# Performance work log

Hardware: AMD Instinct MI355X
Metric: run time of the kernel (lower is better)

## Reference

```python
import jax, jax.numpy as jnp
import numpy as np

B, S, D, H = 8, 1024, 1024, 16
DEPTH = D // H  # 64


def setup_inputs() -> dict:
    key = jax.random.key(0)
    ks = jax.random.split(key, 12)
    s = 1.0 / np.sqrt(D)
    return {
        "Q": jax.random.normal(ks[0], (B, S, D), jnp.float32),
        "K": jax.random.normal(ks[1], (B, S, D), jnp.float32),
        "V": jax.random.normal(ks[2], (B, S, D), jnp.float32),
        "mask": jnp.zeros((B, 1, 1, S), jnp.float32),
        "Wq": jax.random.normal(ks[3], (D, D), jnp.float32) * s,
        "bq": jnp.zeros((D,), jnp.float32),
        "Wk": jax.random.normal(ks[4], (D, D), jnp.float32) * s,
        "bk": jnp.zeros((D,), jnp.float32),
        "Wv": jax.random.normal(ks[5], (D, D), jnp.float32) * s,
        "bv": jnp.zeros((D,), jnp.float32),
        "Wo": jax.random.normal(ks[6], (D, D), jnp.float32) * s,
        "bo": jnp.zeros((D,), jnp.float32),
    }


def _split_heads(x):
    # [B,S,D] -> [B,H,S,depth]
    b, s, _ = x.shape
    return x.reshape(b, s, H, DEPTH).transpose(0, 2, 1, 3)


def reference(Q, K, V, mask, Wq, bq, Wk, bk, Wv, bv, Wo, bo):
    q = _split_heads(Q @ Wq + bq)  # [B,H,S,depth]
    k = _split_heads(K @ Wk + bk)
    v = _split_heads(V @ Wv + bv)
    scale = 1.0 / jnp.sqrt(jnp.asarray(DEPTH, q.dtype))
    scores = jnp.einsum('bhqd,bhkd->bhqk', q, k) * scale  # [B,H,Sq,Sk]
    scores = scores + mask * (-1e9)
    attn = jax.nn.softmax(scores, axis=-1)
    out = jnp.einsum('bhqk,bhkd->bhqd', attn, v)  # [B,H,S,depth]
    out = out.transpose(0, 2, 1, 3).reshape(Q.shape[0], Q.shape[1], D)
    out = out @ Wo + bo
    return out, attn
```

## Files before the change

kernel.cpp:

```cpp
#include <hip/hip_runtime.h>

#define Bb 8
#define Ss 1024
#define Dd 1024
#define Hh 16
#define BSD (Bb*Ss*Dd)
#define DDn (Dd*Dd)

typedef __bf16 bf16x8 __attribute__((ext_vector_type(8)));
typedef float  f32x4  __attribute__((ext_vector_type(4)));

__device__ __forceinline__ unsigned short f2bf(float f){
  unsigned u = __float_as_uint(f);
  u = (u + 0x7fffu + ((u >> 16) & 1u)) >> 16;
  return (unsigned short)u;
}
__device__ __forceinline__ float fexp2(float x){ return __builtin_exp2f(x); }

__device__ __forceinline__ void gload16(const ushort* g, ushort* l){
  __builtin_amdgcn_global_load_lds(
      (const __attribute__((address_space(1))) void*)g,
      (__attribute__((address_space(3))) void*)l, 16, 0, 0);
}

__global__ __launch_bounds__(256) void cvt_bf16(const float4* __restrict__ in,
                                                ushort4* __restrict__ out, int n4){
  int i = blockIdx.x*256 + threadIdx.x;
  if (i >= n4) return;
  float4 v = in[i];
  ushort4 o; o.x = f2bf(v.x); o.y = f2bf(v.y); o.z = f2bf(v.z); o.w = f2bf(v.w);
  out[i] = o;
}

__global__ __launch_bounds__(256) void transpose_w(const float* __restrict__ W,
                                                   ushort* __restrict__ WT){
  __shared__ float tl[32][33];
  int tx = threadIdx.x, ty = threadIdx.y;
  int bx = blockIdx.x*32, by = blockIdx.y*32;
  #pragma unroll
  for (int i=0;i<32;i+=8) tl[ty+i][tx] = W[(by+ty+i)*Dd + bx+tx];
  __syncthreads();
  #pragma unroll
  for (int i=0;i<32;i+=8) WT[(bx+ty+i)*Dd + by+tx] = f2bf(tl[tx][ty+i]);
}

__global__ __launch_bounds__(512) void transpose_v(const ushort* __restrict__ vh,
                                                   ushort* __restrict__ vt){
  __shared__ ushort tl[64][65];
  int tx = threadIdx.x, ty = threadIdx.y;
  long base = (long)blockIdx.y * 65536;
  int s0 = blockIdx.x*64;
  #pragma unroll
  for (int i=0;i<64;i+=8) tl[ty+i][tx] = vh[base + (long)(s0+ty+i)*64 + tx];
  __syncthreads();
  #pragma unroll
  for (int i=0;i<64;i+=8) vt[base + (long)(ty+i)*1024 + s0 + tx] = tl[tx][ty+i];
}

enum { M_PROJ=0, M_FINAL=3 };

template<int MODE>
__global__ __launch_bounds__(256) void gemm128(
    const ushort* __restrict__ A, const ushort* __restrict__ B,
    float* __restrict__ outf, ushort* __restrict__ outh,
    const float* __restrict__ aux)
{
  __shared__ __align__(16) ushort As[128*32];
  __shared__ __align__(16) ushort Bs[128*32];
  const int t = threadIdx.x, lane = t & 63, wave = t >> 6;
  const int m0 = blockIdx.x*128, n0 = blockIdx.y*128;
  const int wm = (wave>>1)*64, wn = (wave&1)*64;
  const int q = lane>>4, l16 = lane&15;
  const int row0 = t>>2, cc = (t&3)*8;

  ushort* lA0 = As + wave*512;
  ushort* lA1 = As + 2048 + wave*512;
  ushort* lB0 = Bs + wave*512;
  ushort* lB1 = Bs + 2048 + wave*512;
  const ushort* gA0 = A + (long)(m0+row0)*Dd + cc;
  const ushort* gA1 = A + (long)(m0+row0+64)*Dd + cc;
  const ushort* gB0 = B + (long)(n0+row0)*Dd + cc;
  const ushort* gB1 = B + (long)(n0+row0+64)*Dd + cc;

  f32x4 acc[4][4] = {};

  for (int k0=0; k0<Dd; k0+=32){
    __syncthreads();
    gload16(gA0+k0, lA0);
    gload16(gA1+k0, lA1);
    gload16(gB0+k0, lB0);
    gload16(gB1+k0, lB1);
    __syncthreads();
    bf16x8 af[4], bfr[4];
    #pragma unroll
    for (int i=0;i<4;i++){
      af[i]  = *(const bf16x8*)(As + (wm+i*16+l16)*32 + q*8);
      bfr[i] = *(const bf16x8*)(Bs + (wn+i*16+l16)*32 + q*8);
    }
    #pragma unroll
    for (int mi=0;mi<4;mi++)
    #pragma unroll
    for (int nj=0;nj<4;nj++)
      acc[mi][nj] = __builtin_amdgcn_mfma_f32_16x16x32_bf16(af[mi],bfr[nj],acc[mi][nj],0,0,0);
  }

  #pragma unroll
  for (int mi=0;mi<4;mi++)
  #pragma unroll
  for (int nj=0;nj<4;nj++)
  #pragma unroll
  for (int r=0;r<4;r++){
    float v = acc[mi][nj][r];
    const int row = m0 + wm + mi*16 + q*4 + r;
    const int col = n0 + wn + nj*16 + l16;
    v += aux[col];
    if (MODE == M_PROJ){
      const int b = row>>10, s = row&1023, h = col>>6, d = col&63;
      outh[((long)((b*Hh + h)*Ss + s)<<6) + d] = f2bf(v);
    } else {
      outf[(long)row*Dd + col] = v;
    }
  }
}

__global__ __launch_bounds__(256) void attn_fused(
    const ushort* __restrict__ qh,
    const ushort* __restrict__ kh,
    const ushort* __restrict__ vt,
    const float*  __restrict__ mask,
    float* __restrict__ attn_f,
    ushort* __restrict__ concat)
{
  __shared__ __align__(16) ushort qs[64][72];
  __shared__ __align__(16) ushort ks[64][72];
  __shared__ __align__(16) ushort vs[64][72];
  __shared__ __align__(16) ushort ps[64][72];
  __shared__ float msk[64];
  __shared__ float red_m[2][64];
  __shared__ float red_l[2][64];

  const int z = blockIdx.z;
  const int b = z >> 4, h = z & 15;
  const int t = threadIdx.x;
  const int lane = t & 63, wave = t >> 6;
  const int wm = (wave >> 1) * 32;
  const int wc = wave & 1;
  const int wn = wc * 32;
  const int q = lane >> 4, l16 = lane & 15;
  const int srow = t >> 2, sc = (t & 3) * 8;

  const ushort* qz = qh + ((long)z << 16);
  const ushort* kz = kh + ((long)z << 16);
  const ushort* vz = vt + ((long)z << 16);
  const int q0 = blockIdx.x * 64;
  const float LOG2E = 1.44269504f;
  const float SC2   = 0.125f * LOG2E;
  const float MSC2  = -1e9f * LOG2E;

  {
    const ushort* src = qz + (long)(q0 + srow) * 64 + sc;
    *(uint4*)(&qs[srow][sc])      = *(const uint4*)(src);
    *(uint4*)(&qs[srow][sc + 32]) = *(const uint4*)(src + 32);
  }

  float m2[2], lsum[2];
  m2[0] = m2[1] = -1e30f; lsum[0] = lsum[1] = 0.f;

  uint4 kv0, kv1; float mv;
  {
    const ushort* ksrc = kz + (long)srow * 64 + sc;
    kv0 = *(const uint4*)(ksrc); kv1 = *(const uint4*)(ksrc + 32);
    mv = (t < 64) ? mask[(b<<10) + t] * MSC2 : 0.f;
  }
  for (int s = 0; s < 16; ++s){
    __syncthreads();
    *(uint4*)(&ks[srow][sc])      = kv0;
    *(uint4*)(&ks[srow][sc + 32]) = kv1;
    if (t < 64) msk[t] = mv;
    __syncthreads();
    if (s < 15){
      const ushort* ksrc = kz + (long)((s+1)*64 + srow) * 64 + sc;
      kv0 = *(const uint4*)(ksrc); kv1 = *(const uint4*)(ksrc + 32);
      if (t < 64) mv = mask[(b<<10) + (s+1)*64 + t] * MSC2;
    }

    f32x4 accs[2][2] = {};
    #pragma unroll
    for (int kk=0; kk<2; ++kk){
      bf16x8 a0 = *(const bf16x8*)(&ks[wm      + l16][kk*32 + q*8]);
      bf16x8 a1 = *(const bf16x8*)(&ks[wm + 16 + l16][kk*32 + q*8]);
      bf16x8 b0 = *(const bf16x8*)(&qs[wn      + l16][kk*32 + q*8]);
      bf16x8 b1 = *(const bf16x8*)(&qs[wn + 16 + l16][kk*32 + q*8]);
      accs[0][0] = __builtin_amdgcn_mfma_f32_16x16x32_bf16(a0,b0,accs[0][0],0,0,0);
      accs[0][1] = __builtin_amdgcn_mfma_f32_16x16x32_bf16(a0,b1,accs[0][1],0,0,0);
      accs[1][0] = __builtin_amdgcn_mfma_f32_16x16x32_bf16(a1,b0,accs[1][0],0,0,0);
      accs[1][1] = __builtin_amdgcn_mfma_f32_16x16x32_bf16(a1,b1,accs[1][1],0,0,0);
    }
    #pragma unroll
    for (int tj=0; tj<2; ++tj){
      float sv[8];
      #pragma unroll
      for (int ti=0; ti<2; ++ti)
      #pragma unroll
      for (int r=0; r<4; ++r){
        const int key = wm + ti*16 + q*4 + r;
        sv[ti*4+r] = accs[ti][tj][r]*SC2 + msk[key];
      }
      float mx01 = fmaxf(sv[0],sv[1]), mx23 = fmaxf(sv[2],sv[3]);
      float mx45 = fmaxf(sv[4],sv[5]), mx67 = fmaxf(sv[6],sv[7]);
      float mx = fmaxf(fmaxf(fmaxf(mx01,mx23), fmaxf(mx45,mx67)), m2[tj]);
      float e0 = fexp2(sv[0]-mx), e1 = fexp2(sv[1]-mx);
      float e2 = fexp2(sv[2]-mx), e3 = fexp2(sv[3]-mx);
      float e4 = fexp2(sv[4]-mx), e5 = fexp2(sv[5]-mx);
      float e6 = fexp2(sv[6]-mx), e7 = fexp2(sv[7]-mx);
      float add = ((e0+e1)+(e2+e3)) + ((e4+e5)+(e6+e7));
      lsum[tj] = lsum[tj]*fexp2(m2[tj]-mx) + add;
      m2[tj] = mx;
    }
  }

  #pragma unroll
  for (int tj=0; tj<2; ++tj){
    float m = m2[tj], l = lsum[tj];
    #pragma unroll
    for (int off=16; off<=32; off<<=1){
      float om = __shfl_xor(m, off, 64);
      float ol = __shfl_xor(l, off, 64);
      float mn = fmaxf(m, om);
      l = l*fexp2(m-mn) + ol*fexp2(om-mn);
      m = mn;
    }
    m2[tj] = m; lsum[tj] = l;
  }
  if (lane < 16){
    #pragma unroll
    for (int tj=0; tj<2; ++tj){
      red_m[wave>>1][wn + tj*16 + l16] = m2[tj];
      red_l[wave>>1][wn + tj*16 + l16] = lsum[tj];
    }
  }
  __syncthreads();
  float m2f[2], li[2];
  #pragma unroll
  for (int tj=0; tj<2; ++tj){
    const int query = wn + tj*16 + l16;
    const float ma = red_m[0][query], mb = red_m[1][query];
    const float la = red_l[0][query], lb = red_l[1][query];
    const float mt = fmaxf(ma, mb);
    m2f[tj] = mt;
    li[tj]  = 1.0f / (la*fexp2(ma-mt) + lb*fexp2(mb-mt));
  }

  f32x4 accp[2][2] = {};
  uint4 vv0, vv1;
  {
    const ushort* ksrc = kz + (long)srow * 64 + sc;
    kv0 = *(const uint4*)(ksrc); kv1 = *(const uint4*)(ksrc + 32);
    const ushort* vsrc = vz + (long)srow * 1024 + sc;
    vv0 = *(const uint4*)(vsrc); vv1 = *(const uint4*)(vsrc + 32);
    mv = (t < 64) ? mask[(b<<10) + t] * MSC2 : 0.f;
  }
  for (int s = 0; s < 16; ++s){
    const int k0 = s * 64;
    __syncthreads();
    *(uint4*)(&ks[srow][sc])      = kv0;
    *(uint4*)(&ks[srow][sc + 32]) = kv1;
    *(uint4*)(&vs[srow][sc])      = vv0;
    *(uint4*)(&vs[srow][sc + 32]) = vv1;
    if (t < 64) msk[t] = mv;
    __syncthreads();
    if (s < 15){
      const ushort* ksrc = kz + (long)(k0 + 64 + srow) * 64 + sc;
      kv0 = *(const uint4*)(ksrc); kv1 = *(const uint4*)(ksrc + 32);
      const ushort* vsrc = vz + (long)srow * 1024 + k0 + 64 + sc;
      vv0 = *(const uint4*)(vsrc); vv1 = *(const uint4*)(vsrc + 32);
      if (t < 64) mv = mask[(b<<10) + k0 + 64 + t] * MSC2;
    }

    f32x4 accs[2][2] = {};
    #pragma unroll
    for (int kk=0; kk<2; ++kk){
      bf16x8 a0 = *(const bf16x8*)(&ks[wm      + l16][kk*32 + q*8]);
      bf16x8 a1 = *(const bf16x8*)(&ks[wm + 16 + l16][kk*32 + q*8]);
      bf16x8 b0 = *(const bf16x8*)(&qs[wn      + l16][kk*32 + q*8]);
      bf16x8 b1 = *(const bf16x8*)(&qs[wn + 16 + l16][kk*32 + q*8]);
      accs[0][0] = __builtin_amdgcn_mfma_f32_16x16x32_bf16(a0,b0,accs[0][0],0,0,0);
      accs[0][1] = __builtin_amdgcn_mfma_f32_16x16x32_bf16(a0,b1,accs[0][1],0,0,0);
      accs[1][0] = __builtin_amdgcn_mfma_f32_16x16x32_bf16(a1,b0,accs[1][0],0,0,0);
      accs[1][1] = __builtin_amdgcn_mfma_f32_16x16x32_bf16(a1,b1,accs[1][1],0,0,0);
    }
    #pragma unroll
    for (int ti=0; ti<2; ++ti)
    #pragma unroll
    for (int tj=0; tj<2; ++tj){
      const int keyb  = wm + ti*16 + q*4;
      const int query = wn + tj*16 + l16;
      float4 pv;
      pv.x = fexp2(accs[ti][tj][0]*SC2 + msk[keyb+0] - m2f[tj]) * li[tj];
      pv.y = fexp2(accs[ti][tj][1]*SC2 + msk[keyb+1] - m2f[tj]) * li[tj];
      pv.z = fexp2(accs[ti][tj][2]*SC2 + msk[keyb+2] - m2f[tj]) * li[tj];
      pv.w = fexp2(accs[ti][tj][3]*SC2 + msk[keyb+3] - m2f[tj]) * li[tj];
      *(float4*)(attn_f + ((long)z<<20) + ((long)(q0+query)<<10) + k0 + keyb) = pv;
      ushort4 pb;
      pb.x = f2bf(pv.x); pb.y = f2bf(pv.y); pb.z = f2bf(pv.z); pb.w = f2bf(pv.w);
      *(ushort4*)(&ps[query][keyb]) = pb;
    }
    __syncthreads();
    #pragma unroll
    for (int kk=0; kk<2; ++kk){
      bf16x8 a0 = *(const bf16x8*)(&ps[wm      + l16][kk*32 + q*8]);
      bf16x8 a1 = *(const bf16x8*)(&ps[wm + 16 + l16][kk*32 + q*8]);
      bf16x8 b0 = *(const bf16x8*)(&vs[wn      + l16][kk*32 + q*8]);
      bf16x8 b1 = *(const bf16x8*)(&vs[wn + 16 + l16][kk*32 + q*8]);
      accp[0][0] = __builtin_amdgcn_mfma_f32_16x16x32_bf16(a0,b0,accp[0][0],0,0,0);
      accp[0][1] = __builtin_amdgcn_mfma_f32_16x16x32_bf16(a0,b1,accp[0][1],0,0,0);
      accp[1][0] = __builtin_amdgcn_mfma_f32_16x16x32_bf16(a1,b0,accp[1][0],0,0,0);
      accp[1][1] = __builtin_amdgcn_mfma_f32_16x16x32_bf16(a1,b1,accp[1][1],0,0,0);
    }
  }

  #pragma unroll
  for (int mi=0; mi<2; mi++)
  #pragma unroll
  for (int nj=0; nj<2; nj++)
  #pragma unroll
  for (int r=0; r<4; r++){
    const int row = q0 + wm + mi*16 + q*4 + r;
    const int d   = wn + nj*16 + l16;
    concat[(((long)(b<<10) + row)<<10) + (h<<6) + d] = f2bf(accp[mi][nj][r]);
  }
}

extern "C" void kernel_launch(void* const* d_in, const int* in_sizes, int n_in,
                              void* d_out, int out_size, void* d_ws, size_t ws_size,
                              hipStream_t stream)
{
  (void)in_sizes; (void)n_in; (void)out_size; (void)ws_size;
  const float* Q    = (const float*)d_in[0];
  const float* Kin  = (const float*)d_in[1];
  const float* V    = (const float*)d_in[2];
  const float* mask = (const float*)d_in[3];
  const float* Wq   = (const float*)d_in[4];
  const float* bq   = (const float*)d_in[5];
  const float* Wk   = (const float*)d_in[6];
  const float* bk   = (const float*)d_in[7];
  const float* Wv   = (const float*)d_in[8];
  const float* bv   = (const float*)d_in[9];
  const float* Wo   = (const float*)d_in[10];
  const float* bo   = (const float*)d_in[11];
  float* out    = (float*)d_out;
  float* attn_f = out + (long)BSD;

  ushort* ws     = (ushort*)d_ws;
  ushort* Xq     = ws;
  ushort* Xk     = Xq  + (long)BSD;
  ushort* Xv     = Xk  + (long)BSD;
  ushort* WqT    = Xv  + (long)BSD;
  ushort* WkT    = WqT + (long)DDn;
  ushort* WvT    = WkT + (long)DDn;
  ushort* WoT    = WvT + (long)DDn;
  ushort* qh     = WoT + (long)DDn;
  ushort* kh     = qh  + (long)BSD;
  ushort* vt     = kh  + (long)BSD;
  ushort* vh     = vt  + (long)BSD;
  ushort* concat = Xq;

  cvt_bf16<<<dim3(BSD/4/256), 256, 0, stream>>>((const float4*)Q,   (ushort4*)Xq, BSD/4);
  cvt_bf16<<<dim3(BSD/4/256), 256, 0, stream>>>((const float4*)Kin, (ushort4*)Xk, BSD/4);
  cvt_bf16<<<dim3(BSD/4/256), 256, 0, stream>>>((const float4*)V,   (ushort4*)Xv, BSD/4);

  transpose_w<<<dim3(32,32), dim3(32,8), 0, stream>>>(Wq, WqT);
  transpose_w<<<dim3(32,32), dim3(32,8), 0, stream>>>(Wk, WkT);
  transpose_w<<<dim3(32,32), dim3(32,8), 0, stream>>>(Wv, WvT);
  transpose_w<<<dim3(32,32), dim3(32,8), 0, stream>>>(Wo, WoT);

  gemm128<M_PROJ><<<dim3(64,8,1), 256, 0, stream>>>(Xq, WqT, nullptr, qh, bq);
  gemm128<M_PROJ><<<dim3(64,8,1), 256, 0, stream>>>(Xk, WkT, nullptr, kh, bk);
  gemm128<M_PROJ><<<dim3(64,8,1), 256, 0, stream>>>(Xv, WvT, nullptr, vh, bv);

  transpose_v<<<dim3(16,128), dim3(64,8), 0, stream>>>(vh, vt);

  attn_fused<<<dim3(16,1,128), 256, 0, stream>>>(qh, kh, vt, mask, attn_f, concat);

  gemm128<M_FINAL><<<dim3(64,8,1), 256, 0, stream>>>(concat, WoT, out, nullptr, bo);
}
```

Measured before the change: 916.9 us.

## Load attention MFMA operands directly from global into registers, drop K/V/Q LDS staging

The attention kernel stops staging Q, K, V and the mask through shared memory. Each wave now loads its own MFMA fragments straight from global memory into registers, with Q held in registers for the whole kernel. The P tile is double-buffered in LDS so only one barrier per iteration remains. This removes LDS round trips and barriers, but each wave re-reads K/V rows that other waves also load, which raises global/L2 traffic and makes the loads less coalesced.

```diff
diff --git a/kernel.cpp b/kernel.cpp
--- a/kernel.cpp
+++ b/kernel.cpp
@@ -131,11 +131,7 @@
     float* __restrict__ attn_f,
     ushort* __restrict__ concat)
 {
-  __shared__ __align__(16) ushort qs[64][72];
-  __shared__ __align__(16) ushort ks[64][72];
-  __shared__ __align__(16) ushort vs[64][72];
-  __shared__ __align__(16) ushort ps[64][72];
-  __shared__ float msk[64];
+  __shared__ __align__(16) ushort ps[2][64][72];
   __shared__ float red_m[2][64];
   __shared__ float red_l[2][64];
 
@@ -147,73 +143,62 @@
   const int wc = wave & 1;
   const int wn = wc * 32;
   const int q = lane >> 4, l16 = lane & 15;
-  const int srow = t >> 2, sc = (t & 3) * 8;
 
   const ushort* qz = qh + ((long)z << 16);
   const ushort* kz = kh + ((long)z << 16);
   const ushort* vz = vt + ((long)z << 16);
+  const float*  mb = mask + (b << 10);
   const int q0 = blockIdx.x * 64;
   const float LOG2E = 1.44269504f;
   const float SC2   = 0.125f * LOG2E;
   const float MSC2  = -1e9f * LOG2E;
 
-  {
-    const ushort* src = qz + (long)(q0 + srow) * 64 + sc;
-    *(uint4*)(&qs[srow][sc])      = *(const uint4*)(src);
-    *(uint4*)(&qs[srow][sc + 32]) = *(const uint4*)(src + 32);
-  }
+  bf16x8 qf[2][2];
+  #pragma unroll
+  for (int tj=0; tj<2; ++tj)
+  #pragma unroll
+  for (int kk=0; kk<2; ++kk)
+    qf[tj][kk] = *(const bf16x8*)(qz + (long)(q0 + wn + tj*16 + l16)*64 + kk*32 + q*8);
 
   float m2[2], lsum[2];
   m2[0] = m2[1] = -1e30f; lsum[0] = lsum[1] = 0.f;
 
-  uint4 kv0, kv1; float mv;
-  {
-    const ushort* ksrc = kz + (long)srow * 64 + sc;
-    kv0 = *(const uint4*)(ksrc); kv1 = *(const uint4*)(ksrc + 32);
-    mv = (t < 64) ? mask[(b<<10) + t] * MSC2 : 0.f;
-  }
+  #pragma unroll 2
   for (int s = 0; s < 16; ++s){
-    __syncthreads();
-    *(uint4*)(&ks[srow][sc])      = kv0;
-    *(uint4*)(&ks[srow][sc + 32]) = kv1;
-    if (t < 64) msk[t] = mv;
-    __syncthreads();
-    if (s < 15){
-      const ushort* ksrc = kz + (long)((s+1)*64 + srow) * 64 + sc;
-      kv0 = *(const uint4*)(ksrc); kv1 = *(const uint4*)(ksrc + 32);
-      if (t < 64) mv = mask[(b<<10) + (s+1)*64 + t] * MSC2;
-    }
+    const int k0 = s * 64;
+    bf16x8 kf0[2], kf1[2];
+    #pragma unroll
+    for (int kk=0; kk<2; ++kk){
+      kf0[kk] = *(const bf16x8*)(kz + (long)(k0 + wm      + l16)*64 + kk*32 + q*8);
+      kf1[kk] = *(const bf16x8*)(kz + (long)(k0 + wm + 16 + l16)*64 + kk*32 + q*8);
+    }
+    const float4 mk0 = *(const float4*)(mb + k0 + wm + q*4);
+    const float4 mk1 = *(const float4*)(mb + k0 + wm + 16 + q*4);
+    float mkv[8];
+    mkv[0]=mk0.x*MSC2; mkv[1]=mk0.y*MSC2; mkv[2]=mk0.z*MSC2; mkv[3]=mk0.w*MSC2;
+    mkv[4]=mk1.x*MSC2; mkv[5]=mk1.y*MSC2; mkv[6]=mk1.z*MSC2; mkv[7]=mk1.w*MSC2;
 
     f32x4 accs[2][2] = {};
     #pragma unroll
     for (int kk=0; kk<2; ++kk){
-      bf16x8 a0 = *(const bf16x8*)(&ks[wm      + l16][kk*32 + q*8]);
-      bf16x8 a1 = *(const bf16x8*)(&ks[wm + 16 + l16][kk*32 + q*8]);
-      bf16x8 b0 = *(const bf16x8*)(&qs[wn      + l16][kk*32 + q*8]);
-      bf16x8 b1 = *(const bf16x8*)(&qs[wn + 16 + l16][kk*32 + q*8]);
-      accs[0][0] = __builtin_amdgcn_mfma_f32_16x16x32_bf16(a0,b0,accs[0][0],0,0,0);
-      accs[0][1] = __builtin_amdgcn_mfma_f32_16x16x32_bf16(a0,b1,accs[0][1],0,0,0);
-      accs[1][0] = __builtin_amdgcn_mfma_f32_16x16x32_bf16(a1,b0,accs[1][0],0,0,0);
-      accs[1][1] = __builtin_amdgcn_mfma_f32_16x16x32_bf16(a1,b1,accs[1][1],0,0,0);
+      accs[0][0] = __builtin_amdgcn_mfma_f32_16x16x32_bf16(kf0[kk],qf[0][kk],accs[0][0],0,0,0);
+      accs[0][1] = __builtin_amdgcn_mfma_f32_16x16x32_bf16(kf0[kk],qf[1][kk],accs[0][1],0,0,0);
+      accs[1][0] = __builtin_amdgcn_mfma_f32_16x16x32_bf16(kf1[kk],qf[0][kk],accs[1][0],0,0,0);
+      accs[1][1] = __builtin_amdgcn_mfma_f32_16x16x32_bf16(kf1[kk],qf[1][kk],accs[1][1],0,0,0);
     }
     #pragma unroll
     for (int tj=0; tj<2; ++tj){
       float sv[8];
       #pragma unroll
-      for (int ti=0; ti<2; ++ti)
-      #pragma unroll
       for (int r=0; r<4; ++r){
-        const int key = wm + ti*16 + q*4 + r;
-        sv[ti*4+r] = accs[ti][tj][r]*SC2 + msk[key];
+        sv[r]   = accs[0][tj][r]*SC2 + mkv[r];
+        sv[4+r] = accs[1][tj][r]*SC2 + mkv[4+r];
       }
       float mx01 = fmaxf(sv[0],sv[1]), mx23 = fmaxf(sv[2],sv[3]);
       float mx45 = fmaxf(sv[4],sv[5]), mx67 = fmaxf(sv[6],sv[7]);
       float mx = fmaxf(fmaxf(fmaxf(mx01,mx23), fmaxf(mx45,mx67)), m2[tj]);
-      float e0 = fexp2(sv[0]-mx), e1 = fexp2(sv[1]-mx);
-      float e2 = fexp2(sv[2]-mx), e3 = fexp2(sv[3]-mx);
-      float e4 = fexp2(sv[4]-mx), e5 = fexp2(sv[5]-mx);
-      float e6 = fexp2(sv[6]-mx), e7 = fexp2(sv[7]-mx);
-      float add = ((e0+e1)+(e2+e3)) + ((e4+e5)+(e6+e7));
+      float add = ((fexp2(sv[0]-mx)+fexp2(sv[1]-mx))+(fexp2(sv[2]-mx)+fexp2(sv[3]-mx)))
+                + ((fexp2(sv[4]-mx)+fexp2(sv[5]-mx))+(fexp2(sv[6]-mx)+fexp2(sv[7]-mx)));
       lsum[tj] = lsum[tj]*fexp2(m2[tj]-mx) + add;
       m2[tj] = mx;
     }
@@ -244,78 +229,70 @@
   #pragma unroll
   for (int tj=0; tj<2; ++tj){
     const int query = wn + tj*16 + l16;
-    const float ma = red_m[0][query], mb = red_m[1][query];
+    const float ma = red_m[0][query], mbv = red_m[1][query];
     const float la = red_l[0][query], lb = red_l[1][query];
-    const float mt = fmaxf(ma, mb);
+    const float mt = fmaxf(ma, mbv);
     m2f[tj] = mt;
-    li[tj]  = 1.0f / (la*fexp2(ma-mt) + lb*fexp2(mb-mt));
+    li[tj]  = 1.0f / (la*fexp2(ma-mt) + lb*fexp2(mbv-mt));
   }
 
   f32x4 accp[2][2] = {};
-  uint4 vv0, vv1;
-  {
-    const ushort* ksrc = kz + (long)srow * 64 + sc;
-    kv0 = *(const uint4*)(ksrc); kv1 = *(const uint4*)(ksrc + 32);
-    const ushort* vsrc = vz + (long)srow * 1024 + sc;
-    vv0 = *(const uint4*)(vsrc); vv1 = *(const uint4*)(vsrc + 32);
-    mv = (t < 64) ? mask[(b<<10) + t] * MSC2 : 0.f;
-  }
+  #pragma unroll 2
   for (int s = 0; s < 16; ++s){
     const int k0 = s * 64;
+    ushort (*psb)[72] = ps[s & 1];
+    bf16x8 kf0[2], kf1[2], vf0[2], vf1[2];
+    #pragma unroll
+    for (int kk=0; kk<2; ++kk){
+      kf0[kk] = *(const bf16x8*)(kz + (long)(k0 + wm      + l16)*64 + kk*32 + q*8);
+      kf1[kk] = *(const bf16x8*)(kz + (long)(k0 + wm + 16 + l16)*64 + kk*32 + q*8);
+      vf0[kk] = *(const bf16x8*)(vz + (long)(wn      + l16)*1024 + k0 + kk*32 + q*8);
+      vf1[kk] = *(const bf16x8*)(vz + (long)(wn + 16 + l16)*1024 + k0 + kk*32 + q*8);
+    }
+    const float4 mk0 = *(const float4*)(mb + k0 + wm + q*4);
+    const float4 mk1 = *(const float4*)(mb + k0 + wm + 16 + q*4);
+    float mkv[8];
+    mkv[0]=mk0.x*MSC2; mkv[1]=mk0.y*MSC2; mkv[2]=mk0.z*MSC2; mkv[3]=mk0.w*MSC2;
+    mkv[4]=mk1.x*MSC2; mkv[5]=mk1.y*MSC2; mkv[6]=mk1.z*MSC2; mkv[7]=mk1.w*MSC2;
+
+    f32x4 accs[2][2] = {};
+    #pragma unroll
+    for (int kk=0; kk<2; ++kk){
+      accs[0][0] = __builtin_amdgcn_mfma_f32_16x16x32_bf16(kf0[kk],qf[0][kk],accs[0][0],0,0,0);
+      accs[0][1] = __builtin_amdgcn_mfma_f32_16x16x32_bf16(kf0[kk],qf[1][kk],accs[0][1],0,0,0);
+      accs[1][0] = __builtin_amdgcn_mfma_f32_16x16x32_bf16(kf1[kk],qf[0][kk],accs[1][0],0,0,0);
+      accs[1][1] = __builtin_amdgcn_mfma_f32_16x16x32_bf16(kf1[kk],qf[1][kk],accs[1][1],0,0,0);
+    }
+    #pragma unroll
+    for (int ti=0; ti<2; ++ti){
+      const int keyb = wm + ti*16 + q*4;
+      #pragma unroll
+      for (int tj=0; tj<2; ++tj){
+        const int query = wn + tj*16 + l16;
+        float4 pv;
+        pv.x = fexp2(accs[ti][tj][0]*SC2 + mkv[ti*4+0] - m2f[tj]) * li[tj];
+        pv.y = fexp2(accs[ti][tj][1]*SC2 + mkv[ti*4+1] - m2f[tj]) * li[tj];
+        pv.z = fexp2(accs[ti][tj][2]*SC2 + mkv[ti*4+2] - m2f[tj]) * li[tj];
+        pv.w = fexp2(accs[ti][tj][3]*SC2 + mkv[ti*4+3] - m2f[tj]) * li[tj];
+        *(float4*)(attn_f + ((long)z<<20) + ((long)(q0+query)<<10) + k0 + keyb) = pv;
+        ushort4 pb;
+        pb.x = f2bf(pv.x); pb.y = f2bf(pv.y); pb.z = f2bf(pv.z); pb.w = f2bf(pv.w);
+        *(ushort4*)(&psb[query][keyb]) = pb;
+      }
+    }
     __syncthreads();
-    *(uint4*)(&ks[srow][sc])      = kv0;
-    *(uint4*)(&ks[srow][sc + 32]) = kv1;
-    *(uint4*)(&vs[srow][sc])      = vv0;
-    *(uint4*)(&vs[srow][sc + 32]) = vv1;
-    if (t < 64) msk[t] = mv;
-    __syncthreads();
-    if (s < 15){
-      const ushort* ksrc = kz + (long)(k0 + 64 + srow) * 64 + sc;
-      kv0 = *(const uint4*)(ksrc); kv1 = *(const uint4*)(ksrc + 32);
-      const ushort* vsrc = vz + (long)srow * 1024 + k0 + 64 + sc;
-      vv0 = *(const uint4*)(vsrc); vv1 = *(const uint4*)(vsrc + 32);
-      if (t < 64) mv = mask[(b<<10) + k0 + 64 + t] * MSC2;
-    }
-
-    f32x4 accs[2][2] = {};
-    #pragma unroll
-    for (int kk=0; kk<2; ++kk){
-      bf16x8 a0 = *(const bf16x8*)(&ks[wm      + l16][kk*32 + q*8]);
-      bf16x8 a1 = *(const bf16x8*)(&ks[wm + 16 + l16][kk*32 + q*8]);
-      bf16x8 b0 = *(const bf16x8*)(&qs[wn      + l16][kk*32 + q*8]);
-      bf16x8 b1 = *(const bf16x8*)(&qs[wn + 16 + l16][kk*32 + q*8]);
-      accs[0][0] = __builtin_amdgcn_mfma_f32_16x16x32_bf16(a0,b0,accs[0][0],0,0,0);
-      accs[0][1] = __builtin_amdgcn_mfma_f32_16x16x32_bf16(a0,b1,accs[0][1],0,0,0);
-      accs[1][0] = __builtin_amdgcn_mfma_f32_16x16x32_bf16(a1,b0,accs[1][0],0,0,0);
-      accs[1][1] = __builtin_amdgcn_mfma_f32_16x16x32_bf16(a1,b1,accs[1][1],0,0,0);
-    }
-    #pragma unroll
-    for (int ti=0; ti<2; ++ti)
-    #pragma unroll
-    for (int tj=0; tj<2; ++tj){
-      const int keyb  = wm + ti*16 + q*4;
-      const int query = wn + tj*16 + l16;
-      float4 pv;
-      pv.x = fexp2(accs[ti][tj][0]*SC2 + msk[keyb+0] - m2f[tj]) * li[tj];
-      pv.y = fexp2(accs[ti][tj][1]*SC2 + msk[keyb+1] - m2f[tj]) * li[tj];
-      pv.z = fexp2(accs[ti][tj][2]*SC2 + msk[keyb+2] - m2f[tj]) * li[tj];
-      pv.w = fexp2(accs[ti][tj][3]*SC2 + msk[keyb+3] - m2f[tj]) * li[tj];
-      *(float4*)(attn_f + ((long)z<<20) + ((long)(q0+query)<<10) + k0 + keyb) = pv;
-      ushort4 pb;
-      pb.x = f2bf(pv.x); pb.y = f2bf(pv.y); pb.z = f2bf(pv.z); pb.w = f2bf(pv.w);
-      *(ushort4*)(&ps[query][keyb]) = pb;
-    }
-    __syncthreads();
-    #pragma unroll
-    for (int kk=0; kk<2; ++kk){
-      bf16x8 a0 = *(const bf16x8*)(&ps[wm      + l16][kk*32 + q*8]);
-      bf16x8 a1 = *(const bf16x8*)(&ps[wm + 16 + l16][kk*32 + q*8]);
-      bf16x8 b0 = *(const bf16x8*)(&vs[wn      + l16][kk*32 + q*8]);
-      bf16x8 b1 = *(const bf16x8*)(&vs[wn + 16 + l16][kk*32 + q*8]);
-      accp[0][0] = __builtin_amdgcn_mfma_f32_16x16x32_bf16(a0,b0,accp[0][0],0,0,0);
-      accp[0][1] = __builtin_amdgcn_mfma_f32_16x16x32_bf16(a0,b1,accp[0][1],0,0,0);
-      accp[1][0] = __builtin_amdgcn_mfma_f32_16x16x32_bf16(a1,b0,accp[1][0],0,0,0);
-      accp[1][1] = __builtin_amdgcn_mfma_f32_16x16x32_bf16(a1,b1,accp[1][1],0,0,0);
+    bf16x8 pa0[2], pa1[2];
+    #pragma unroll
+    for (int kk=0; kk<2; ++kk){
+      pa0[kk] = *(const bf16x8*)(&psb[wm      + l16][kk*32 + q*8]);
+      pa1[kk] = *(const bf16x8*)(&psb[wm + 16 + l16][kk*32 + q*8]);
+    }
+    #pragma unroll
+    for (int kk=0; kk<2; ++kk){
+      accp[0][0] = __builtin_amdgcn_mfma_f32_16x16x32_bf16(pa0[kk],vf0[kk],accp[0][0],0,0,0);
+      accp[0][1] = __builtin_amdgcn_mfma_f32_16x16x32_bf16(pa0[kk],vf1[kk],accp[0][1],0,0,0);
+      accp[1][0] = __builtin_amdgcn_mfma_f32_16x16x32_bf16(pa1[kk],vf0[kk],accp[1][0],0,0,0);
+      accp[1][1] = __builtin_amdgcn_mfma_f32_16x16x32_bf16(pa1[kk],vf1[kk],accp[1][1],0,0,0);
     }
   }
 
```

After: 969.6 us. 5.7% more time.
